# Kernel optimization log

Hardware: AMD Instinct MI355X
Metric: run time of the kernel (lower is better)

Reference implementation:

```python
import jax, jax.numpy as jnp
import numpy as np

T, B, S, D, H = 1024, 2, 4096, 1024, 16  # queries, batch, kv_len, embed_dim, heads
HD = D // H


def setup_inputs() -> dict:
    key = jax.random.key(0)
    ks = jax.random.split(key, 12)
    f = lambda k, sh: jax.random.normal(k, sh, dtype=jnp.float32)
    w = lambda k: f(k, (D, D)) * 0.02  # torch Linear weight [out, in]
    return {
        "hidden_states": f(ks[0], (T, B, D)),
        "attention_mask": f(ks[1], (B * H, T, S)),
        "position_embeddings": f(ks[2], (T, B, D)),
        "key_value_states": f(ks[3], (S, B, D)),
        "key_value_position_embeddings": f(ks[4], (S, B, D)),
        "Wq": w(ks[5]), "bq": jnp.zeros((D,), jnp.float32),
        "Wk": w(ks[6]), "bk": jnp.zeros((D,), jnp.float32),
        "Wv": w(ks[7]), "bv": jnp.zeros((D,), jnp.float32),
        "Wo": w(ks[8]), "bo": jnp.zeros((D,), jnp.float32),
    }


def reference(hidden_states, attention_mask, position_embeddings,
              key_value_states, key_value_position_embeddings,
              Wq, bq, Wk, bk, Wv, bv, Wo, bo):
    # inputs are [seq, batch, dim]; module permutes to [batch, seq, dim]
    hs = jnp.transpose(hidden_states, (1, 0, 2))            # [B, T, D]
    pos = jnp.transpose(position_embeddings, (1, 0, 2))      # [B, T, D]
    kv = jnp.transpose(key_value_states, (1, 0, 2))          # [B, S, D]
    kvpos = jnp.transpose(key_value_position_embeddings, (1, 0, 2))
    b, t, d = hs.shape
    s = kv.shape[1]
    hd = d // H
    scaling = hd ** -0.5

    q = ((hs + pos) @ Wq.T + bq) * scaling                   # pos-embed added to q
    k = (kv + kvpos) @ Wk.T + bk                             # pos-embed added to k
    v = kv @ Wv.T + bv                                       # v from original kv

    q = q.reshape(b, t, H, hd).transpose(0, 2, 1, 3)         # [B, H, T, hd]
    k = k.reshape(b, s, H, hd).transpose(0, 2, 1, 3)         # [B, H, S, hd]
    v = v.reshape(b, s, H, hd).transpose(0, 2, 1, 3)         # [B, H, S, hd]

    scores = jnp.einsum('bhtd,bhsd->bhts', q, k)             # [B, H, T, S]
    scores = scores + attention_mask.reshape(b, H, t, s)
    probs = jax.nn.softmax(scores, axis=-1)                  # dropout p=0.0 -> identity

    ctx = jnp.einsum('bhts,bhsd->bhtd', probs, v)            # [B, H, T, hd]
    ctx = ctx.transpose(0, 2, 1, 3).reshape(b, t, d)         # [B, T, D]
    out = ctx @ Wo.T + bo
    return jnp.transpose(out, (1, 0, 2))                     # back to [T, B, D]
```

## Files before the change

kernel.cpp:

```cpp
#include <hip/hip_runtime.h>
#include <stdint.h>

typedef __attribute__((ext_vector_type(8))) short short8;
typedef __attribute__((ext_vector_type(4))) float f32x4;
typedef __attribute__((ext_vector_type(4))) unsigned short u16x4;

__device__ __forceinline__ unsigned short f2bf(float x){
  union { float f; unsigned int u; } v; v.f = x;
  unsigned int r = v.u + 0x7fffu + ((v.u >> 16) & 1u);
  return (unsigned short)(r >> 16);
}

__device__ __forceinline__ f32x4 mfma16(short8 a, short8 b, f32x4 c){
  return __builtin_amdgcn_mfma_f32_16x16x32_bf16(a, b, c, 0, 0, 0);
}

__device__ __forceinline__ void async16(const void* g, void* l){
  __builtin_amdgcn_global_load_lds(
      (__attribute__((address_space(1))) void*)g,
      (__attribute__((address_space(3))) void*)l, 16, 0, 0);
}

__device__ __forceinline__ u16x4 cvt4(float4 x){
  u16x4 r; r.x = f2bf(x.x); r.y = f2bf(x.y); r.z = f2bf(x.z); r.w = f2bf(x.w);
  return r;
}

__global__ __launch_bounds__(256) void k_prep_all(
    const float4* __restrict__ hs, const float4* __restrict__ pos,
    const float4* __restrict__ kv, const float4* __restrict__ kvpos,
    const float4* __restrict__ Wq, const float4* __restrict__ Wk,
    const float4* __restrict__ Wv, const float4* __restrict__ Wo,
    u16x4* __restrict__ Aq, u16x4* __restrict__ Ak, u16x4* __restrict__ Av,
    u16x4* __restrict__ Wqb, u16x4* __restrict__ Wkb,
    u16x4* __restrict__ Wvb, u16x4* __restrict__ Wob)
{
  int i = blockIdx.x * 256 + threadIdx.x;
  if (i < 524288){
    float4 a = hs[i], b = pos[i];
    a.x += b.x; a.y += b.y; a.z += b.z; a.w += b.w;
    Aq[i] = cvt4(a);
  } else if (i < 2621440){
    int j = i - 524288;
    float4 a = kv[j], b = kvpos[j];
    Av[j] = cvt4(a);
    a.x += b.x; a.y += b.y; a.z += b.z; a.w += b.w;
    Ak[j] = cvt4(a);
  } else if (i < 2883584){
    int j = i - 2621440; Wqb[j] = cvt4(Wq[j]);
  } else if (i < 3145728){
    int j = i - 2883584; Wkb[j] = cvt4(Wk[j]);
  } else if (i < 3407872){
    int j = i - 3145728; Wvb[j] = cvt4(Wv[j]);
  } else {
    int j = i - 3407872; Wob[j] = cvt4(Wo[j]);
  }
}

template<int MODE>
__global__ __launch_bounds__(256,2) void k_gemm(const unsigned short* __restrict__ A,
    const unsigned short* __restrict__ W, const float* __restrict__ bias,
    void* __restrict__ outp, int M, float scale)
{
  __shared__ unsigned short lA[128*32];
  __shared__ unsigned short lB[128*32];
  const int tid = threadIdx.x, lane = tid & 63, w = tid >> 6;
  const int quad = lane >> 4, m16 = lane & 15;
  const int wm = w & 1, wn = w >> 1;
  const int row0 = blockIdx.x * 128, col0 = blockIdx.y * 128;
  const int g0 = w*64 + lane, g1 = (w+4)*64 + lane;
  const int r0g = g0 & 127, q0g = g0 >> 7;
  const int r1g = g1 & 127, q1g = g1 >> 7;
  const unsigned short* Ab = A + (size_t)row0 * 1024;
  const unsigned short* Bb = W + (size_t)col0 * 1024;
  f32x4 acc[4][4] = {};
  for (int k0 = 0; k0 < 1024; k0 += 32){
    async16(Ab + (size_t)r0g*1024 + k0 + q0g*8, &lA[w*512]);
    async16(Ab + (size_t)r1g*1024 + k0 + q1g*8, &lA[(w+4)*512]);
    async16(Bb + (size_t)r0g*1024 + k0 + q0g*8, &lB[w*512]);
    async16(Bb + (size_t)r1g*1024 + k0 + q1g*8, &lB[(w+4)*512]);
    __syncthreads();
    short8 af[4], bfr[4];
    #pragma unroll
    for (int mt = 0; mt < 4; ++mt)
      af[mt] = *(const short8*)&lA[(quad*128 + wm*64 + mt*16 + m16)*8];
    #pragma unroll
    for (int nt = 0; nt < 4; ++nt)
      bfr[nt] = *(const short8*)&lB[(quad*128 + wn*64 + nt*16 + m16)*8];
    #pragma unroll
    for (int mt = 0; mt < 4; ++mt)
      #pragma unroll
      for (int nt = 0; nt < 4; ++nt)
        acc[mt][nt] = mfma16(af[mt], bfr[nt], acc[mt][nt]);
    __syncthreads();
  }
  if (MODE == 0){
    unsigned short* out16 = (unsigned short*)outp;
    const int SEQ = M >> 1;
    #pragma unroll
    for (int nt = 0; nt < 4; ++nt){
      const int n = col0 + wn*64 + nt*16 + m16;
      const float bvv = bias[n];
      const int h = n >> 6, d = n & 63;
      #pragma unroll
      for (int mt = 0; mt < 4; ++mt){
        const int rbase = row0 + wm*64 + mt*16 + quad*4;
        #pragma unroll
        for (int r = 0; r < 4; ++r){
          const int rr = rbase + r;
          const int seq = rr >> 1, bb = rr & 1;
          const float vv = (acc[mt][nt][r] + bvv) * scale;
          out16[(((size_t)(bb*16 + h) * SEQ + seq) << 6) + d] = f2bf(vv);
        }
      }
    }
  } else if (MODE == 1){
    float* outf = (float*)outp;
    #pragma unroll
    for (int nt = 0; nt < 4; ++nt){
      const int n = col0 + wn*64 + nt*16 + m16;
      const float bvv = bias[n];
      #pragma unroll
      for (int mt = 0; mt < 4; ++mt){
        const int rbase = row0 + wm*64 + mt*16 + quad*4;
        #pragma unroll
        for (int r = 0; r < 4; ++r){
          const int rr = rbase + r;
          const int tt = rr & 1023, bb = rr >> 10;
          outf[(((size_t)tt*2 + bb) << 10) + n] = acc[mt][nt][r] + bvv;
        }
      }
    }
  } else {
    unsigned short* out16 = (unsigned short*)outp;
    #pragma unroll
    for (int nt = 0; nt < 4; ++nt){
      const int n = col0 + wn*64 + nt*16 + m16;
      const float bvv = bias[n];
      const int h = n >> 6, d = n & 63;
      #pragma unroll
      for (int mt = 0; mt < 4; ++mt){
        const int rbase = row0 + wm*64 + mt*16 + quad*4;
        #pragma unroll
        for (int r = 0; r < 4; ++r){
          const int rr = rbase + r;
          const int seq = rr >> 1, bb = rr & 1;
          out16[(((size_t)((bb*16 + h)*64 + d)) << 12) + seq] = f2bf(acc[mt][nt][r] + bvv);
        }
      }
    }
  }
}

__global__ __launch_bounds__(256,2) void k_flash(const unsigned short* __restrict__ Qp,
    const unsigned short* __restrict__ Kp, const unsigned short* __restrict__ VTp,
    const float* __restrict__ mask, unsigned short* __restrict__ ctx)
{
  __shared__ unsigned short pl[4096];
  const int tid = threadIdx.x, lane = tid & 63, w = tid >> 6;
  const int quad = lane >> 4, m16 = lane & 15;
  const int bh = blockIdx.x >> 4;
  const int t0 = ((blockIdx.x & 15) << 6) + w*16;
  short8 qa0, qa1;
  {
    const unsigned short* qp = Qp + (((size_t)bh*1024 + t0 + m16) << 6) + quad*8;
    qa0 = *(const short8*)qp;
    qa1 = *(const short8*)(qp + 32);
  }
  const unsigned short* kb = Kp + (((size_t)bh*4096 + m16) << 6) + quad*8;
  const unsigned short* vb = VTp + (((size_t)(bh*64 + m16)) << 12) + quad*8;
  const float* mb = mask + ((size_t)bh*1024 + t0 + quad*4) * 4096 + m16;
  unsigned short* pw = &pl[w*1024];
  const unsigned short* prd0 = &pl[w*1024 + (quad*16 + (m16 ^ quad))*8];
  const unsigned short* prd1 = &pl[w*1024 + ((quad+4)*16 + (m16 ^ (quad+4)))*8];
  f32x4 Oa[4] = {};
  float mrow[4], lrow[4];
  #pragma unroll
  for (int r = 0; r < 4; ++r){ mrow[r] = -1e30f; lrow[r] = 0.f; }
  const f32x4 zero4 = {0.f, 0.f, 0.f, 0.f};

  short8 kA[8], kB[8];
  float mA[16], mB[16];

  auto LK = [&](int s0, short8* kf){
    #pragma unroll
    for (int c = 0; c < 4; ++c){
      const unsigned short* kp = kb + ((size_t)(s0 + c*16) << 6);
      kf[2*c]   = *(const short8*)kp;
      kf[2*c+1] = *(const short8*)(kp + 32);
    }
  };
  auto LM = [&](int s0, float* mf){
    const float* mp = mb + s0;
    #pragma unroll
    for (int c = 0; c < 4; ++c)
      #pragma unroll
      for (int r = 0; r < 4; ++r)
        mf[c*4+r] = __builtin_nontemporal_load(mp + (size_t)r*4096 + c*16);
  };
  auto PROC = [&](int s0, const short8* kf, const float* mf){
    f32x4 sc[4];
    #pragma unroll
    for (int c = 0; c < 4; ++c){
      f32x4 z = mfma16(qa0, kf[2*c], zero4);
      sc[c] = mfma16(qa1, kf[2*c+1], z);
    }
    short8 vf[8];
    #pragma unroll
    for (int cn = 0; cn < 4; ++cn){
      const unsigned short* vp = vb + ((size_t)cn << 16) + s0;
      vf[2*cn]   = *(const short8*)vp;
      vf[2*cn+1] = *(const short8*)(vp + 32);
    }
    #pragma unroll
    for (int c = 0; c < 4; ++c)
      #pragma unroll
      for (int r = 0; r < 4; ++r)
        sc[c][r] += mf[c*4+r];
    float rmax[4];
    #pragma unroll
    for (int r = 0; r < 4; ++r)
      rmax[r] = fmaxf(fmaxf(sc[0][r], sc[1][r]), fmaxf(sc[2][r], sc[3][r]));
    #pragma unroll
    for (int off = 1; off <= 8; off <<= 1)
      #pragma unroll
      for (int r = 0; r < 4; ++r)
        rmax[r] = fmaxf(rmax[r], __shfl_xor(rmax[r], off, 64));
    float al[4], rsum[4];
    #pragma unroll
    for (int r = 0; r < 4; ++r){
      float mn = fmaxf(mrow[r], rmax[r]);
      al[r] = __expf(mrow[r] - mn);
      mrow[r] = mn;
      rsum[r] = 0.f;
    }
    #pragma unroll
    for (int c = 0; c < 4; ++c)
      #pragma unroll
      for (int r = 0; r < 4; ++r){
        float p = __expf(sc[c][r] - mrow[r]);
        sc[c][r] = p;
        rsum[r] += p;
      }
    #pragma unroll
    for (int off = 1; off <= 8; off <<= 1)
      #pragma unroll
      for (int r = 0; r < 4; ++r)
        rsum[r] += __shfl_xor(rsum[r], off, 64);
    #pragma unroll
    for (int r = 0; r < 4; ++r)
      lrow[r] = lrow[r]*al[r] + rsum[r];
    #pragma unroll
    for (int cn = 0; cn < 4; ++cn)
      #pragma unroll
      for (int r = 0; r < 4; ++r)
        Oa[cn][r] *= al[r];
    #pragma unroll
    for (int c = 0; c < 4; ++c){
      const int kch = c*2 + (m16 >> 3);
      #pragma unroll
      for (int r = 0; r < 4; ++r){
        const int row = quad*4 + r;
        pw[(kch*16 + (row ^ kch))*8 + (m16 & 7)] = f2bf(sc[c][r]);
      }
    }
    asm volatile("s_waitcnt lgkmcnt(0)" ::: "memory");
    short8 pa0 = *(const short8*)prd0;
    short8 pa1 = *(const short8*)prd1;
    #pragma unroll
    for (int cn = 0; cn < 4; ++cn){
      Oa[cn] = mfma16(pa0, vf[2*cn], Oa[cn]);
      Oa[cn] = mfma16(pa1, vf[2*cn+1], Oa[cn]);
    }
  };

  LK(0, kA); LM(0, mA);
  for (int s0 = 0; s0 < 4096; s0 += 128){
    LK(s0+64, kB); LM(s0+64, mB);
    PROC(s0, kA, mA);
    if (s0 + 128 < 4096){ LK(s0+128, kA); LM(s0+128, mA); }
    PROC(s0+64, kB, mB);
  }

  const int b = bh >> 4, h = bh & 15;
  unsigned short* op = ctx + (((size_t)b*1024 + t0 + quad*4) << 10) + h*64 + m16;
  #pragma unroll
  for (int r = 0; r < 4; ++r){
    float inv = 1.f / lrow[r];
    #pragma unroll
    for (int cn = 0; cn < 4; ++cn)
      op[((size_t)r << 10) + cn*16] = f2bf(Oa[cn][r]*inv);
  }
}

extern "C" void kernel_launch(void* const* d_in, const int* in_sizes, int n_in,
                              void* d_out, int out_size, void* d_ws, size_t ws_size,
                              hipStream_t stream)
{
  (void)in_sizes; (void)n_in; (void)out_size; (void)ws_size;
  const float* hs    = (const float*)d_in[0];
  const float* mask  = (const float*)d_in[1];
  const float* pos   = (const float*)d_in[2];
  const float* kv    = (const float*)d_in[3];
  const float* kvpos = (const float*)d_in[4];
  const float* Wq = (const float*)d_in[5];  const float* biq = (const float*)d_in[6];
  const float* Wk = (const float*)d_in[7];  const float* bik = (const float*)d_in[8];
  const float* Wv = (const float*)d_in[9];  const float* biv = (const float*)d_in[10];
  const float* Wo = (const float*)d_in[11]; const float* bio = (const float*)d_in[12];
  float* out = (float*)d_out;
  char* ws = (char*)d_ws;
  unsigned short* Aq  = (unsigned short*)(ws + ( 0ull << 20));
  unsigned short* Ak  = (unsigned short*)(ws + ( 4ull << 20));
  unsigned short* Av  = (unsigned short*)(ws + (20ull << 20));
  unsigned short* Wqb = (unsigned short*)(ws + (36ull << 20));
  unsigned short* Wkb = (unsigned short*)(ws + (38ull << 20));
  unsigned short* Wvb = (unsigned short*)(ws + (40ull << 20));
  unsigned short* Wob = (unsigned short*)(ws + (42ull << 20));
  unsigned short* Qb  = (unsigned short*)(ws + (44ull << 20));
  unsigned short* Kb  = (unsigned short*)(ws + (48ull << 20));
  unsigned short* VTb = (unsigned short*)(ws + (64ull << 20));
  unsigned short* ctx = (unsigned short*)(ws + (36ull << 20));

  k_prep_all<<<dim3(14336), dim3(256), 0, stream>>>(
      (const float4*)hs, (const float4*)pos, (const float4*)kv, (const float4*)kvpos,
      (const float4*)Wq, (const float4*)Wk, (const float4*)Wv, (const float4*)Wo,
      (u16x4*)Aq, (u16x4*)Ak, (u16x4*)Av,
      (u16x4*)Wqb, (u16x4*)Wkb, (u16x4*)Wvb, (u16x4*)Wob);

  k_gemm<0><<<dim3(16, 8), dim3(256), 0, stream>>>(Aq, Wqb, biq, Qb, 2048, 0.125f);
  k_gemm<0><<<dim3(64, 8), dim3(256), 0, stream>>>(Ak, Wkb, bik, Kb, 8192, 1.0f);
  k_gemm<2><<<dim3(64, 8), dim3(256), 0, stream>>>(Av, Wvb, biv, VTb, 8192, 1.0f);
  k_flash<<<dim3(512), dim3(256), 0, stream>>>(Qb, Kb, VTb, mask, ctx);
  k_gemm<1><<<dim3(16, 8), dim3(256), 0, stream>>>(ctx, Wob, bio, out, 2048, 1.0f);
}
```

Measured before the change: 1.051 ms.

## Stage K/V tiles through LDS with async loads and use exp2 softmax

```diff
diff --git a/kernel.cpp b/kernel.cpp
--- a/kernel.cpp
+++ b/kernel.cpp
@@ -20,6 +20,12 @@
       (__attribute__((address_space(1))) void*)g,
       (__attribute__((address_space(3))) void*)l, 16, 0, 0);
 }
+
+#if __has_builtin(__builtin_amdgcn_exp2f)
+__device__ __forceinline__ float exp2_fast(float x){ return __builtin_amdgcn_exp2f(x); }
+#else
+__device__ __forceinline__ float exp2_fast(float x){ return __expf(x * 0.69314718f); }
+#endif
 
 __device__ __forceinline__ u16x4 cvt4(float4 x){
   u16x4 r; r.x = f2bf(x.x); r.y = f2bf(x.y); r.z = f2bf(x.z); r.w = f2bf(x.w);
@@ -156,6 +162,8 @@
     const unsigned short* __restrict__ Kp, const unsigned short* __restrict__ VTp,
     const float* __restrict__ mask, unsigned short* __restrict__ ctx)
 {
+  __shared__ unsigned short lK0[4096], lK1[4096];
+  __shared__ unsigned short lV0[4096], lV1[4096];
   __shared__ unsigned short pl[4096];
   const int tid = threadIdx.x, lane = tid & 63, w = tid >> 6;
   const int quad = lane >> 4, m16 = lane & 15;
@@ -167,28 +175,30 @@
     qa0 = *(const short8*)qp;
     qa1 = *(const short8*)(qp + 32);
   }
-  const unsigned short* kb = Kp + (((size_t)bh*4096 + m16) << 6) + quad*8;
-  const unsigned short* vb = VTp + (((size_t)(bh*64 + m16)) << 12) + quad*8;
+  const unsigned short* Kbh = Kp + ((size_t)bh << 18);
+  const unsigned short* Vbh = VTp + ((size_t)bh << 18);
   const float* mb = mask + ((size_t)bh*1024 + t0 + quad*4) * 4096 + m16;
   unsigned short* pw = &pl[w*1024];
   const unsigned short* prd0 = &pl[w*1024 + (quad*16 + (m16 ^ quad))*8];
   const unsigned short* prd1 = &pl[w*1024 + ((quad+4)*16 + (m16 ^ (quad+4)))*8];
+
+  const int sr = tid >> 3;
+  const int sk = (tid & 7) ^ (sr & 7);
+  const int swzlo = quad ^ (m16 & 7);
+  const int swzhi = swzlo ^ 4;
+
   f32x4 Oa[4] = {};
   float mrow[4], lrow[4];
   #pragma unroll
   for (int r = 0; r < 4; ++r){ mrow[r] = -1e30f; lrow[r] = 0.f; }
   const f32x4 zero4 = {0.f, 0.f, 0.f, 0.f};
-
-  short8 kA[8], kB[8];
   float mA[16], mB[16];
 
-  auto LK = [&](int s0, short8* kf){
-    #pragma unroll
-    for (int c = 0; c < 4; ++c){
-      const unsigned short* kp = kb + ((size_t)(s0 + c*16) << 6);
-      kf[2*c]   = *(const short8*)kp;
-      kf[2*c+1] = *(const short8*)(kp + 32);
-    }
+  auto STAGE = [&](int s0, unsigned short* dK, unsigned short* dV){
+    async16(Kbh + (size_t)(s0 + sr)*64 + sk*8,        dK + w*512);
+    async16(Kbh + (size_t)(s0 + 32 + sr)*64 + sk*8,   dK + 2048 + w*512);
+    async16(Vbh + (size_t)sr*4096 + s0 + sk*8,        dV + w*512);
+    async16(Vbh + (size_t)(32 + sr)*4096 + s0 + sk*8, dV + 2048 + w*512);
   };
   auto LM = [&](int s0, float* mf){
     const float* mp = mb + s0;
@@ -198,25 +208,32 @@
       for (int r = 0; r < 4; ++r)
         mf[c*4+r] = __builtin_nontemporal_load(mp + (size_t)r*4096 + c*16);
   };
-  auto PROC = [&](int s0, const short8* kf, const float* mf){
+  auto PROC = [&](const unsigned short* Kt, const unsigned short* Vt, const float* mf){
+    short8 kf[8];
+    #pragma unroll
+    for (int c = 0; c < 4; ++c){
+      const unsigned short* kp = Kt + (c*128 + m16*8)*8;
+      kf[2*c]   = *(const short8*)(kp + swzlo*8);
+      kf[2*c+1] = *(const short8*)(kp + swzhi*8);
+    }
+    short8 vf[8];
+    #pragma unroll
+    for (int cn = 0; cn < 4; ++cn){
+      const unsigned short* vp = Vt + (cn*128 + m16*8)*8;
+      vf[2*cn]   = *(const short8*)(vp + swzlo*8);
+      vf[2*cn+1] = *(const short8*)(vp + swzhi*8);
+    }
     f32x4 sc[4];
     #pragma unroll
     for (int c = 0; c < 4; ++c){
       f32x4 z = mfma16(qa0, kf[2*c], zero4);
       sc[c] = mfma16(qa1, kf[2*c+1], z);
     }
-    short8 vf[8];
-    #pragma unroll
-    for (int cn = 0; cn < 4; ++cn){
-      const unsigned short* vp = vb + ((size_t)cn << 16) + s0;
-      vf[2*cn]   = *(const short8*)vp;
-      vf[2*cn+1] = *(const short8*)(vp + 32);
-    }
     #pragma unroll
     for (int c = 0; c < 4; ++c)
       #pragma unroll
       for (int r = 0; r < 4; ++r)
-        sc[c][r] += mf[c*4+r];
+        sc[c][r] = fmaf(mf[c*4+r], 1.44269504f, sc[c][r]);
     float rmax[4];
     #pragma unroll
     for (int r = 0; r < 4; ++r)
@@ -230,7 +247,7 @@
     #pragma unroll
     for (int r = 0; r < 4; ++r){
       float mn = fmaxf(mrow[r], rmax[r]);
-      al[r] = __expf(mrow[r] - mn);
+      al[r] = exp2_fast(mrow[r] - mn);
       mrow[r] = mn;
       rsum[r] = 0.f;
     }
@@ -238,7 +255,7 @@
     for (int c = 0; c < 4; ++c)
       #pragma unroll
       for (int r = 0; r < 4; ++r){
-        float p = __expf(sc[c][r] - mrow[r]);
+        float p = exp2_fast(sc[c][r] - mrow[r]);
         sc[c][r] = p;
         rsum[r] += p;
       }
@@ -274,12 +291,16 @@
     }
   };
 
-  LK(0, kA); LM(0, mA);
+  STAGE(0, lK0, lV0); LM(0, mA);
+  asm volatile("s_waitcnt vmcnt(0)" ::: "memory");
+  __syncthreads();
   for (int s0 = 0; s0 < 4096; s0 += 128){
-    LK(s0+64, kB); LM(s0+64, mB);
-    PROC(s0, kA, mA);
-    if (s0 + 128 < 4096){ LK(s0+128, kA); LM(s0+128, mA); }
-    PROC(s0+64, kB, mB);
+    STAGE(s0+64, lK1, lV1); LM(s0+64, mB);
+    PROC(lK0, lV0, mA);
+    __syncthreads();
+    if (s0 + 128 < 4096){ STAGE(s0+128, lK0, lV0); LM(s0+128, mA); }
+    PROC(lK1, lV1, mB);
+    __syncthreads();
   }
 
   const int b = bh >> 4, h = bh & 15;
@@ -327,7 +348,7 @@
       (u16x4*)Aq, (u16x4*)Ak, (u16x4*)Av,
       (u16x4*)Wqb, (u16x4*)Wkb, (u16x4*)Wvb, (u16x4*)Wob);
 
-  k_gemm<0><<<dim3(16, 8), dim3(256), 0, stream>>>(Aq, Wqb, biq, Qb, 2048, 0.125f);
+  k_gemm<0><<<dim3(16, 8), dim3(256), 0, stream>>>(Aq, Wqb, biq, Qb, 2048, 0.18033688f);
   k_gemm<0><<<dim3(64, 8), dim3(256), 0, stream>>>(Ak, Wkb, bik, Kb, 8192, 1.0f);
   k_gemm<2><<<dim3(64, 8), dim3(256), 0, stream>>>(Av, Wvb, biv, VTb, 8192, 1.0f);
   k_flash<<<dim3(512), dim3(256), 0, stream>>>(Qb, Kb, VTb, mask, ctx);
```

After: 946.5 us. -9.9%, faster.
